# Performance work log

Hardware: AMD Instinct MI355X
Metric: run time of the kernel (lower is better)

Reference implementation:

```python
import jax, jax.numpy as jnp
import numpy as np
import math

FACTOR = 5  # Informer 'factor' hyperparameter


def setup_inputs() -> dict:
    key = jax.random.key(0)
    B, L, H, D = 2, 2048, 16, 128
    k1, k2, k3, k4 = jax.random.split(key, 4)
    queries = jax.random.normal(k1, (B, L, H, D), jnp.float32)
    keys = jax.random.normal(k2, (B, L, H, D), jnp.float32)
    values = jax.random.normal(k3, (B, L, H, D), jnp.float32)
    sample_k = max(1, min(FACTOR * math.ceil(math.log(L)), L))  # u in the paper
    index_sample = jax.random.randint(k4, (L, sample_k), 0, L, dtype=jnp.int32)
    return {"queries": queries, "keys": keys, "values": values,
            "index_sample": index_sample}


def reference(queries, keys, values, index_sample):
    # queries/keys/values: [B, L, H, D] -> [B, H, L, D]
    Q = jnp.swapaxes(queries, 1, 2)
    K = jnp.swapaxes(keys, 1, 2)
    V = jnp.swapaxes(values, 1, 2)
    B, H, L_Q, D = Q.shape
    L_K = K.shape[2]
    # U_part = factor*ceil(ln L_K), clipped to L_K then to L_Q (n_top in _prob_QK)
    n_top = max(1, min(FACTOR * math.ceil(math.log(L_K)), L_K, L_Q))

    # --- _prob_QK: sampled scores ---
    # K_sample: [B, H, L_Q, sample_k, D] (same materialization as torch K_expand gather)
    K_sample = K[:, :, index_sample, :]
    Q_K_sample = jnp.einsum('bhqd,bhqsd->bhqs', Q, K_sample)
    # sparsity measure M: max - mean(over full L_K, per original torch code)
    M = Q_K_sample.max(axis=-1) - Q_K_sample.sum(axis=-1) / L_K  # [B,H,L_Q]
    _, M_top = jax.lax.top_k(M, n_top)  # [B,H,n_top]

    # gather top queries and compute their full attention rows
    Q_reduce = jnp.take_along_axis(Q, M_top[..., None], axis=2)  # [B,H,u,D]
    scores = jnp.einsum('bhud,bhkd->bhuk', Q_reduce, K)  # [B,H,u,L_K]
    scale = 1.0 / math.sqrt(D)
    scores = scores * scale

    # --- initial context (mask_flag=False): mean of V over keys ---
    context = jnp.broadcast_to(V.mean(axis=2, keepdims=True), (B, H, L_Q, D))

    # --- update context at top-query positions ---
    attn = jax.nn.softmax(scores, axis=-1)
    upd = jnp.einsum('bhuk,bhkd->bhud', attn, V)  # [B,H,u,D]
    bi = jnp.arange(B)[:, None, None]
    hi = jnp.arange(H)[None, :, None]
    context = context.at[bi, hi, M_top].set(upd)

    return jnp.swapaxes(context, 1, 2)  # [B, L_Q, H, D]
```

## Files before the change

kernel.cpp:

```cpp
#include <hip/hip_runtime.h>
#include <math.h>

#define B_    2
#define L_    2048
#define H_    16
#define D_    128
#define S_    40
#define NTOP_ 40
#define NCH_  8
#define CHK_  256
#define VCH_  32

#define SCALE_ 0.08838834764831843f

#define NVP_BLKS   1024
#define NSAMP_BLKS 16384

__global__ __launch_bounds__(256) void k1_sample_vpart(const float* __restrict__ Q,
                                                       const float* __restrict__ K,
                                                       const float* __restrict__ V,
                                                       const int* __restrict__ idx,
                                                       float* __restrict__ M,
                                                       float* __restrict__ vpart,
                                                       int* __restrict__ cnt) {
    const int bid = blockIdx.x;
    const int t   = threadIdx.x;

    if (bid < NVP_BLKS) {
        __shared__ float red[256];
        if (bid == 0 && t < 32) cnt[t] = 0;
        const int vbid = bid;
        const int bh  = vbid >> 5;
        const int lc  = vbid & (VCH_ - 1);
        const int h   = bh & (H_ - 1);
        const int b   = bh >> 4;
        const int d   = t & (D_ - 1);
        const int sub = t >> 7;
        float acc = 0.0f;
        const int l0 = lc * (L_ / VCH_);
        for (int l = l0 + sub; l < l0 + L_ / VCH_; l += 2)
            acc += V[((size_t)(b * L_ + l) * H_ + h) * D_ + d];
        red[t] = acc;
        __syncthreads();
        if (t < D_) vpart[(size_t)vbid * D_ + t] = red[t] + red[t + 128];
        return;
    }

    const int sb   = bid - NVP_BLKS;
    const int xcd  = sb & 7;
    const int li   = sb >> 3;
    const int bh   = (xcd << 2) + (li >> 9);
    const int rb   = li & 511;
    const int wave = t >> 6;
    const int lane = t & 63;
    const int q    = rb * 4 + wave;
    const int h    = bh & (H_ - 1);
    const int b    = bh >> 4;
    const int g    = lane >> 3;
    const int sub  = lane & 7;

    const float4* Q4 = (const float4*)Q;
    const float4* K4 = (const float4*)K;
    const size_t rowQ = ((size_t)(b * L_ + q) * H_ + h) * 32;
    const size_t kbase = ((size_t)b * L_ * H_ + h) * 32 + sub;
    const int* ip = idx + q * S_;

    int kidx[5];
    #pragma unroll
    for (int s = 0; s < 5; ++s) kidx[s] = ip[s * 8 + g];

    const float4 qv0 = Q4[rowQ + 0  + sub];
    const float4 qv1 = Q4[rowQ + 8  + sub];
    const float4 qv2 = Q4[rowQ + 16 + sub];
    const float4 qv3 = Q4[rowQ + 24 + sub];

    float4 kv[5][4];
    #pragma unroll
    for (int s = 0; s < 5; ++s) {
        const float4* kb = K4 + kbase + (size_t)kidx[s] * (H_ * 32);
        kv[s][0] = kb[0];
        kv[s][1] = kb[8];
        kv[s][2] = kb[16];
        kv[s][3] = kb[24];
    }
    __builtin_amdgcn_sched_barrier(0);

    float smax = -INFINITY, ssum = 0.0f;
    #pragma unroll
    for (int s = 0; s < 5; ++s) {
        float p = qv0.x * kv[s][0].x + qv0.y * kv[s][0].y + qv0.z * kv[s][0].z + qv0.w * kv[s][0].w
                + qv1.x * kv[s][1].x + qv1.y * kv[s][1].y + qv1.z * kv[s][1].z + qv1.w * kv[s][1].w
                + qv2.x * kv[s][2].x + qv2.y * kv[s][2].y + qv2.z * kv[s][2].z + qv2.w * kv[s][2].w
                + qv3.x * kv[s][3].x + qv3.y * kv[s][3].y + qv3.z * kv[s][3].z + qv3.w * kv[s][3].w;
        p += __shfl_xor(p, 1);
        p += __shfl_xor(p, 2);
        p += __shfl_xor(p, 4);
        smax = fmaxf(smax, p);
        ssum += p;
    }
    #pragma unroll
    for (int o = 8; o < 64; o <<= 1) {
        smax = fmaxf(smax, __shfl_xor(smax, o));
        ssum += __shfl_xor(ssum, o);
    }
    if (lane == 0) M[(size_t)bh * L_ + q] = smax - ssum * (1.0f / L_);
}

__global__ __launch_bounds__(256) void k2_rank_fill(const float* __restrict__ M,
                                                    const float* __restrict__ vpart,
                                                    int* __restrict__ cnt,
                                                    int* __restrict__ topk,
                                                    float* __restrict__ out) {
    __shared__ unsigned int ue[L_];
    __shared__ int hist[256], sscan[256];
    __shared__ int eqlist[256];
    __shared__ int sh_chosen, sh_need, sh_eqcnt;
    __shared__ float mlf[256];
    const int bid = blockIdx.x;
    const int t   = threadIdx.x;

    if (bid < 32) {
        const int bh = bid;
        const float* Mrow = M + (size_t)bh * L_;
        for (int i = t; i < L_; i += 256) {
            const unsigned int ub = __float_as_uint(Mrow[i]);
            ue[i] = (ub & 0x80000000u) ? ~ub : (ub | 0x80000000u);
        }
        if (t == 0) sh_eqcnt = 0;
        __syncthreads();

        unsigned int prefix = 0;
        int need = NTOP_;
        for (int l = 3; l >= 0; --l) {
            hist[t] = 0;
            __syncthreads();
            for (int i = t; i < L_; i += 256) {
                const unsigned int u = ue[i];
                const bool match = (l == 3) || ((u >> (8 * (l + 1))) == prefix);
                if (match) atomicAdd(&hist[(u >> (8 * l)) & 255], 1);
            }
            __syncthreads();
            sscan[t] = hist[t];
            __syncthreads();
            for (int off = 1; off < 256; off <<= 1) {
                const int v = (t + off < 256) ? sscan[t + off] : 0;
                __syncthreads();
                sscan[t] += v;
                __syncthreads();
            }
            const int above = sscan[t] - hist[t];
            if (above < need && need <= above + hist[t]) {
                sh_chosen = t;
                sh_need = need - above;
            }
            __syncthreads();
            prefix = (prefix << 8) | (unsigned int)sh_chosen;
            need = sh_need;
            __syncthreads();
        }
        const unsigned int T40 = prefix;
        const int rem = need;

        for (int i = t; i < L_; i += 256) {
            const unsigned int u = ue[i];
            if (u > T40) {
                const int pos = atomicAdd(&cnt[bh], 1);
                topk[bh * NTOP_ + pos] = i;
            } else if (u == T40) {
                const int p = atomicAdd(&sh_eqcnt, 1);
                if (p < 256) eqlist[p] = i;
            }
        }
        __syncthreads();
        const int n = min(sh_eqcnt, 256);
        for (int i = t; i < n; i += 256) {
            const int mye = eqlist[i];
            int rk = 0;
            for (int j = 0; j < n; ++j) rk += (eqlist[j] < mye);
            if (rk < rem) {
                const int pos = atomicAdd(&cnt[bh], 1);
                topk[bh * NTOP_ + pos] = mye;
            }
        }
    } else {
        const int fb = bid - 32;
        const int bh = fb >> 6;
        const int sl = fb & 63;
        const int h  = bh & (H_ - 1);
        const int b  = bh >> 4;
        const int d    = t & (D_ - 1);
        const int half = t >> 7;
        float s = 0.0f;
        #pragma unroll
        for (int c = half * 16; c < half * 16 + 16; ++c)
            s += vpart[(size_t)(bh * VCH_ + c) * D_ + d];
        mlf[t] = s;
        __syncthreads();
        if (t < D_) mlf[t] = (mlf[t] + mlf[t + 128]) * (1.0f / L_);
        __syncthreads();
        const float4 vm4 = *(const float4*)&mlf[(t & 31) * 4];
        float4* out4 = (float4*)out;
        const int q0 = sl * 32;
        #pragma unroll
        for (int k = 0; k < 4; ++k) {
            const int j = k * 256 + t;
            const int r = j >> 5;
            out4[((size_t)(b * L_ + q0 + r) * H_ + h) * 32 + (t & 31)] = vm4;
        }
    }
}

__global__ __launch_bounds__(256) void k_scorepv(const float* __restrict__ Q,
                                                 const float* __restrict__ K,
                                                 const float* __restrict__ V,
                                                 const int* __restrict__ topk,
                                                 float* __restrict__ pmax,
                                                 float* __restrict__ psum,
                                                 float* __restrict__ pout) {
    __shared__ float Qs[20 * D_];
    __shared__ float S[20 * 260];
    __shared__ float Ks[64 * 132];
    __shared__ float mrow[20];
    __shared__ int   tq[20];
    const int bid = blockIdx.x;
    const int xcd = bid & 7;
    const int loc = bid >> 3;
    const int bh  = (xcd << 2) + (loc >> 4);
    const int sub16 = loc & 15;
    const int kc  = sub16 >> 1;
    const int uh  = sub16 & 1;
    const int h   = bh & (H_ - 1);
    const int b   = bh >> 4;
    const int t   = threadIdx.x;

    if (t < 20) tq[t] = topk[bh * NTOP_ + uh * 20 + t];
    __syncthreads();

    {
        const float4* Q4 = (const float4*)Q;
        float4* Qs4 = (float4*)Qs;
        #pragma unroll
        for (int it = 0; it < 3; ++it) {
            const int i = it * 256 + t;
            if (i < 640) {
                const int u = i >> 5, dc = i & 31;
                Qs4[i] = Q4[((size_t)(b * L_ + tq[u]) * H_ + h) * 32 + dc];
            }
        }
    }
    __syncthreads();

    {
        const float4* K4 = (const float4*)K;
        const float4* Qs4 = (const float4*)Qs;
        float4* Ks4 = (float4*)Ks;
        const int r = t & 63, uq = t >> 6;
        for (int pass = 0; pass < 4; ++pass) {
            #pragma unroll
            for (int j = 0; j < 8; ++j) {
                const int gidx = j * 256 + t;
                const int row = gidx >> 5, c = gidx & 31;
                Ks4[row * 33 + c] =
                    K4[((size_t)(b * L_ + kc * CHK_ + pass * 64 + row) * H_ + h) * 32 + c];
            }
            __syncthreads();
            float acc[5] = {0.f, 0.f, 0.f, 0.f, 0.f};
            for (int dc = 0; dc < 32; ++dc) {
                const float4 kv = Ks4[r * 33 + dc];
                #pragma unroll
                for (int u5 = 0; u5 < 5; ++u5) {
                    const float4 qv = Qs4[(uq * 5 + u5) * 32 + dc];
                    acc[u5] += qv.x * kv.x + qv.y * kv.y + qv.z * kv.z + qv.w * kv.w;
                }
            }
            #pragma unroll
            for (int u5 = 0; u5 < 5; ++u5)
                S[(uq * 5 + u5) * 260 + pass * 64 + r] = acc[u5] * SCALE_;
            __syncthreads();
        }
    }

    {
        const int w = t >> 6, lane = t & 63;
        #pragma unroll
        for (int uu = 0; uu < 5; ++uu) {
            const int u = w * 5 + uu;
            const float* Sr = S + u * 260;
            float v = fmaxf(fmaxf(Sr[lane], Sr[lane + 64]),
                            fmaxf(Sr[lane + 128], Sr[lane + 192]));
            #pragma unroll
            for (int o = 1; o < 64; o <<= 1) v = fmaxf(v, __shfl_xor(v, o, 64));
            if (lane == 0) mrow[u] = v;
        }
    }
    __syncthreads();

    #pragma unroll
    for (int u = 0; u < 20; ++u) S[u * 260 + t] = __expf(S[u * 260 + t] - mrow[u]);
    __syncthreads();

    {
        const int w = t >> 6, lane = t & 63;
        #pragma unroll
        for (int uu = 0; uu < 5; ++uu) {
            const int u = w * 5 + uu;
            const float* Sr = S + u * 260;
            float v = Sr[lane] + Sr[lane + 64] + Sr[lane + 128] + Sr[lane + 192];
            #pragma unroll
            for (int o = 1; o < 64; o <<= 1) v += __shfl_xor(v, o, 64);
            if (lane == 0) {
                psum[(bh * NCH_ + kc) * NTOP_ + uh * 20 + u] = v;
                pmax[(bh * NCH_ + kc) * NTOP_ + uh * 20 + u] = mrow[u];
            }
        }
    }

    {
        const int d  = t & (D_ - 1);
        const int g  = t >> 7;
        const int u0 = g * 10;
        float acc2[10];
        #pragma unroll
        for (int u = 0; u < 10; ++u) acc2[u] = 0.0f;
        const float* Vb = V + ((size_t)(b * L_ + kc * CHK_) * H_ + h) * D_ + d;
        for (int kq = 0; kq < CHK_ / 4; ++kq) {
            const float v0 = Vb[(size_t)(kq * 4 + 0) * (H_ * D_)];
            const float v1 = Vb[(size_t)(kq * 4 + 1) * (H_ * D_)];
            const float v2 = Vb[(size_t)(kq * 4 + 2) * (H_ * D_)];
            const float v3 = Vb[(size_t)(kq * 4 + 3) * (H_ * D_)];
            #pragma unroll
            for (int u = 0; u < 10; ++u) {
                const float4 p = *(const float4*)&S[(u0 + u) * 260 + kq * 4];
                acc2[u] += p.x * v0 + p.y * v1 + p.z * v2 + p.w * v3;
            }
        }
        float* pb = pout + (((size_t)(bh * NCH_ + kc)) * NTOP_ + uh * 20 + u0) * D_ + d;
        #pragma unroll
        for (int u = 0; u < 10; ++u) pb[(size_t)u * D_] = acc2[u];
    }
}

__global__ __launch_bounds__(128) void k_comb(const float* __restrict__ pmax,
                                              const float* __restrict__ psum,
                                              const float* __restrict__ pout,
                                              const int* __restrict__ topk,
                                              float* __restrict__ out) {
    const int bid = blockIdx.x;
    const int bh  = bid / NTOP_;
    const int u   = bid - bh * NTOP_;
    const int h   = bh & (H_ - 1);
    const int b   = bh >> 4;
    const int t   = threadIdx.x;

    float pm[NCH_];
    float M = -INFINITY;
    #pragma unroll
    for (int c = 0; c < NCH_; ++c) {
        pm[c] = pmax[(bh * NCH_ + c) * NTOP_ + u];
        M = fmaxf(M, pm[c]);
    }
    float ssum = 0.0f, o = 0.0f;
    #pragma unroll
    for (int c = 0; c < NCH_; ++c) {
        const float w = __expf(pm[c] - M);
        ssum += psum[(bh * NCH_ + c) * NTOP_ + u] * w;
        o += pout[((size_t)(bh * NCH_ + c) * NTOP_ + u) * D_ + t] * w;
    }
    const int qi = topk[bh * NTOP_ + u];
    out[((size_t)(b * L_ + qi) * H_ + h) * D_ + t] = o / ssum;
}

extern "C" void kernel_launch(void* const* d_in, const int* in_sizes, int n_in,
                              void* d_out, int out_size, void* d_ws, size_t ws_size,
                              hipStream_t stream) {
    const float* Q  = (const float*)d_in[0];
    const float* K  = (const float*)d_in[1];
    const float* V  = (const float*)d_in[2];
    const int* idx  = (const int*)d_in[3];
    float* out      = (float*)d_out;

    char* ws = (char*)d_ws;
    size_t off = 0;
    float* Mws   = (float*)(ws + off); off += (size_t)65536 * 4;
    float* vpart = (float*)(ws + off); off += (size_t)1024 * 128 * 4;
    int*   cnt   = (int*)(ws + off);   off += 32 * 4;
    int*   topk  = (int*)(ws + off);   off += 1280 * 4;
    float* pmax  = (float*)(ws + off); off += (size_t)256 * 40 * 4;
    float* psum  = (float*)(ws + off); off += (size_t)256 * 40 * 4;
    float* pout  = (float*)(ws + off); off += (size_t)256 * 40 * 128 * 4;

    hipLaunchKernelGGL(k1_sample_vpart, dim3(NVP_BLKS + NSAMP_BLKS), dim3(256), 0, stream,
                       Q, K, V, idx, Mws, vpart, cnt);
    hipLaunchKernelGGL(k2_rank_fill,    dim3(32 + 2048), dim3(256), 0, stream,
                       Mws, vpart, cnt, topk, out);
    hipLaunchKernelGGL(k_scorepv,       dim3(512),  dim3(256), 0, stream,
                       Q, K, V, topk, pmax, psum, pout);
    hipLaunchKernelGGL(k_comb,          dim3(1280), dim3(128), 0, stream,
                       pmax, psum, pout, topk, out);
}
```

Before: 135.8 us.

## Score sampled keys in bf16, then refine top-k candidates with exact fp32

```diff
diff --git a/kernel.cpp b/kernel.cpp
--- a/kernel.cpp
+++ b/kernel.cpp
@@ -10,81 +10,157 @@
 #define NCH_  8
 #define CHK_  256
 #define VCH_  32
+#define CAND_ 512
 
 #define SCALE_ 0.08838834764831843f
 
-#define NVP_BLKS   1024
-#define NSAMP_BLKS 16384
-
-__global__ __launch_bounds__(256) void k1_sample_vpart(const float* __restrict__ Q,
-                                                       const float* __restrict__ K,
-                                                       const float* __restrict__ V,
-                                                       const int* __restrict__ idx,
-                                                       float* __restrict__ M,
-                                                       float* __restrict__ vpart,
-                                                       int* __restrict__ cnt) {
-    const int bid = blockIdx.x;
+__device__ __forceinline__ unsigned int encf(float f) {
+    unsigned int u = __float_as_uint(f);
+    return (u & 0x80000000u) ? ~u : (u | 0x80000000u);
+}
+__device__ __forceinline__ float decf(unsigned int e) {
+    unsigned int u = (e & 0x80000000u) ? (e ^ 0x80000000u) : ~e;
+    return __uint_as_float(u);
+}
+__device__ __forceinline__ unsigned int bfpack(float a, float b) {
+    unsigned int ua = __float_as_uint(a); ua = (ua + 0x7fffu + ((ua >> 16) & 1u)) >> 16;
+    unsigned int ub = __float_as_uint(b); ub = (ub + 0x7fffu + ((ub >> 16) & 1u)) >> 16;
+    return ua | (ub << 16);
+}
+__device__ __forceinline__ float lo16(unsigned int u) { return __uint_as_float(u << 16); }
+__device__ __forceinline__ float hi16(unsigned int u) { return __uint_as_float(u & 0xffff0000u); }
+
+__global__ __launch_bounds__(256) void kpack(const float* __restrict__ K,
+                                             unsigned int* __restrict__ Kbf) {
+    const int bid = blockIdx.x, t = threadIdx.x;
+    const int bh = bid >> 3, kc = bid & 7;
+    const int h = bh & 15, b = bh >> 4;
+    const float4* K4 = (const float4*)K;
+    uint2* out2 = (uint2*)Kbf;
+    for (int j = 0; j < 32; ++j) {
+        const int g = j * 256 + t;
+        const int row = g >> 5, c = g & 31;
+        const float4 v = K4[((size_t)(b * L_ + kc * 256 + row) * H_ + h) * 32 + c];
+        out2[(size_t)(bh * L_ + kc * 256 + row) * 32 + c] =
+            make_uint2(bfpack(v.x, v.y), bfpack(v.z, v.w));
+    }
+}
+
+__global__ __launch_bounds__(256) void k0_vpart(const float* __restrict__ V,
+                                                float* __restrict__ vpart) {
+    __shared__ float red[256];
+    const int vbid = blockIdx.x;
+    const int bh  = vbid >> 5;
+    const int lc  = vbid & (VCH_ - 1);
+    const int h   = bh & 15, b = bh >> 4;
     const int t   = threadIdx.x;
-
-    if (bid < NVP_BLKS) {
-        __shared__ float red[256];
-        if (bid == 0 && t < 32) cnt[t] = 0;
-        const int vbid = bid;
-        const int bh  = vbid >> 5;
-        const int lc  = vbid & (VCH_ - 1);
-        const int h   = bh & (H_ - 1);
-        const int b   = bh >> 4;
-        const int d   = t & (D_ - 1);
-        const int sub = t >> 7;
-        float acc = 0.0f;
-        const int l0 = lc * (L_ / VCH_);
-        for (int l = l0 + sub; l < l0 + L_ / VCH_; l += 2)
-            acc += V[((size_t)(b * L_ + l) * H_ + h) * D_ + d];
-        red[t] = acc;
-        __syncthreads();
-        if (t < D_) vpart[(size_t)vbid * D_ + t] = red[t] + red[t + 128];
-        return;
-    }
-
-    const int sb   = bid - NVP_BLKS;
+    const int d   = t & (D_ - 1);
+    const int sub = t >> 7;
+    float acc = 0.0f;
+    const int l0 = lc * (L_ / VCH_);
+    for (int l = l0 + sub; l < l0 + L_ / VCH_; l += 2)
+        acc += V[((size_t)(b * L_ + l) * H_ + h) * D_ + d];
+    red[t] = acc;
+    __syncthreads();
+    if (t < D_) vpart[(size_t)vbid * D_ + t] = red[t] + red[t + 128];
+}
+
+__global__ __launch_bounds__(256) void k1_sample_bf16(const float* __restrict__ Q,
+                                                      const uint4* __restrict__ KB,
+                                                      const int* __restrict__ idx,
+                                                      float* __restrict__ M) {
+    const int sb   = blockIdx.x;
     const int xcd  = sb & 7;
     const int li   = sb >> 3;
     const int bh   = (xcd << 2) + (li >> 9);
     const int rb   = li & 511;
-    const int wave = t >> 6;
-    const int lane = t & 63;
+    const int wave = threadIdx.x >> 6, lane = threadIdx.x & 63;
     const int q    = rb * 4 + wave;
-    const int h    = bh & (H_ - 1);
-    const int b    = bh >> 4;
-    const int g    = lane >> 3;
-    const int sub  = lane & 7;
+    const int h    = bh & 15, b = bh >> 4;
+    const int g    = lane >> 3, sub = lane & 7;
+
+    const float4* Q4 = (const float4*)Q;
+    const size_t rowQ = ((size_t)(b * L_ + q) * H_ + h) * 32;
+    const int* ip = idx + q * S_;
+    int kidx[5];
+    #pragma unroll
+    for (int s = 0; s < 5; ++s) kidx[s] = ip[s * 8 + g];
+
+    const float4 qa0 = Q4[rowQ + 2 * sub];
+    const float4 qa1 = Q4[rowQ + 2 * sub + 1];
+    const float4 qb0 = Q4[rowQ + 16 + 2 * sub];
+    const float4 qb1 = Q4[rowQ + 16 + 2 * sub + 1];
+
+    uint4 kv[5][2];
+    #pragma unroll
+    for (int s = 0; s < 5; ++s) {
+        const uint4* kr = KB + ((size_t)bh * L_ + kidx[s]) * 16;
+        kv[s][0] = kr[sub];
+        kv[s][1] = kr[8 + sub];
+    }
+    __builtin_amdgcn_sched_barrier(0);
+
+    float smax = -INFINITY, ssum = 0.0f;
+    #pragma unroll
+    for (int s = 0; s < 5; ++s) {
+        float p = 0.f;
+        {
+            const uint4 u = kv[s][0];
+            p += qa0.x * lo16(u.x) + qa0.y * hi16(u.x) + qa0.z * lo16(u.y) + qa0.w * hi16(u.y);
+            p += qa1.x * lo16(u.z) + qa1.y * hi16(u.z) + qa1.z * lo16(u.w) + qa1.w * hi16(u.w);
+        }
+        {
+            const uint4 u = kv[s][1];
+            p += qb0.x * lo16(u.x) + qb0.y * hi16(u.x) + qb0.z * lo16(u.y) + qb0.w * hi16(u.y);
+            p += qb1.x * lo16(u.z) + qb1.y * hi16(u.z) + qb1.z * lo16(u.w) + qb1.w * hi16(u.w);
+        }
+        p += __shfl_xor(p, 1);
+        p += __shfl_xor(p, 2);
+        p += __shfl_xor(p, 4);
+        smax = fmaxf(smax, p);
+        ssum += p;
+    }
+    #pragma unroll
+    for (int o = 8; o < 64; o <<= 1) {
+        smax = fmaxf(smax, __shfl_xor(smax, o));
+        ssum += __shfl_xor(ssum, o);
+    }
+    if (lane == 0) M[(size_t)bh * L_ + q] = smax - ssum * (1.0f / L_);
+}
+
+__global__ __launch_bounds__(256) void k1_sample_f32(const float* __restrict__ Q,
+                                                     const float* __restrict__ K,
+                                                     const int* __restrict__ idx,
+                                                     float* __restrict__ M) {
+    const int sb   = blockIdx.x;
+    const int xcd  = sb & 7;
+    const int li   = sb >> 3;
+    const int bh   = (xcd << 2) + (li >> 9);
+    const int rb   = li & 511;
+    const int wave = threadIdx.x >> 6, lane = threadIdx.x & 63;
+    const int q    = rb * 4 + wave;
+    const int h    = bh & 15, b = bh >> 4;
+    const int g    = lane >> 3, sub = lane & 7;
 
     const float4* Q4 = (const float4*)Q;
     const float4* K4 = (const float4*)K;
     const size_t rowQ = ((size_t)(b * L_ + q) * H_ + h) * 32;
     const size_t kbase = ((size_t)b * L_ * H_ + h) * 32 + sub;
     const int* ip = idx + q * S_;
-
     int kidx[5];
     #pragma unroll
     for (int s = 0; s < 5; ++s) kidx[s] = ip[s * 8 + g];
-
-    const float4 qv0 = Q4[rowQ + 0  + sub];
-    const float4 qv1 = Q4[rowQ + 8  + sub];
+    const float4 qv0 = Q4[rowQ + 0 + sub];
+    const float4 qv1 = Q4[rowQ + 8 + sub];
     const float4 qv2 = Q4[rowQ + 16 + sub];
     const float4 qv3 = Q4[rowQ + 24 + sub];
-
     float4 kv[5][4];
     #pragma unroll
     for (int s = 0; s < 5; ++s) {
         const float4* kb = K4 + kbase + (size_t)kidx[s] * (H_ * 32);
-        kv[s][0] = kb[0];
-        kv[s][1] = kb[8];
-        kv[s][2] = kb[16];
-        kv[s][3] = kb[24];
+        kv[s][0] = kb[0]; kv[s][1] = kb[8]; kv[s][2] = kb[16]; kv[s][3] = kb[24];
     }
     __builtin_amdgcn_sched_barrier(0);
-
     float smax = -INFINITY, ssum = 0.0f;
     #pragma unroll
     for (int s = 0; s < 5; ++s) {
@@ -106,106 +182,133 @@
     if (lane == 0) M[(size_t)bh * L_ + q] = smax - ssum * (1.0f / L_);
 }
 
-__global__ __launch_bounds__(256) void k2_rank_fill(const float* __restrict__ M,
-                                                    const float* __restrict__ vpart,
-                                                    int* __restrict__ cnt,
-                                                    int* __restrict__ topk,
-                                                    float* __restrict__ out) {
-    __shared__ unsigned int ue[L_];
-    __shared__ int hist[256], sscan[256];
-    __shared__ int eqlist[256];
-    __shared__ int sh_chosen, sh_need, sh_eqcnt;
-    __shared__ float mlf[256];
-    const int bid = blockIdx.x;
-    const int t   = threadIdx.x;
-
+__global__ __launch_bounds__(1024) void k2_rank_refine_fill(const float* __restrict__ Mws,
+                                                            const float* __restrict__ Q,
+                                                            const float* __restrict__ K,
+                                                            const int* __restrict__ idx,
+                                                            const float* __restrict__ vpart,
+                                                            int* __restrict__ topk,
+                                                            float* __restrict__ out,
+                                                            float delta) {
+    const int bid = blockIdx.x, t = threadIdx.x;
     if (bid < 32) {
-        const int bh = bid;
-        const float* Mrow = M + (size_t)bh * L_;
-        for (int i = t; i < L_; i += 256) {
-            const unsigned int ub = __float_as_uint(Mrow[i]);
-            ue[i] = (ub & 0x80000000u) ? ~ub : (ub | 0x80000000u);
-        }
-        if (t == 0) sh_eqcnt = 0;
-        __syncthreads();
-
-        unsigned int prefix = 0;
-        int need = NTOP_;
+        __shared__ unsigned int ue[L_];
+        __shared__ int hist[256], sscan[256];
+        __shared__ int sh_chosen, sh_need, sh_nc;
+        __shared__ int clist[CAND_];
+        __shared__ float cMx[CAND_];
+        __shared__ unsigned int cmaxe[CAND_];
+        __shared__ float csum[CAND_];
+        const int bh = bid, h = bh & 15, b = bh >> 4;
+        const float* Mrow = Mws + (size_t)bh * L_;
+        for (int i = t; i < L_; i += 1024) ue[i] = encf(Mrow[i]);
+        if (t == 0) sh_nc = 0;
+        __syncthreads();
+
+        unsigned int prefix = 0; int need = NTOP_;
         for (int l = 3; l >= 0; --l) {
-            hist[t] = 0;
-            __syncthreads();
-            for (int i = t; i < L_; i += 256) {
+            if (t < 256) hist[t] = 0;
+            __syncthreads();
+            for (int i = t; i < L_; i += 1024) {
                 const unsigned int u = ue[i];
                 const bool match = (l == 3) || ((u >> (8 * (l + 1))) == prefix);
                 if (match) atomicAdd(&hist[(u >> (8 * l)) & 255], 1);
             }
             __syncthreads();
-            sscan[t] = hist[t];
+            if (t < 256) sscan[t] = hist[t];
             __syncthreads();
             for (int off = 1; off < 256; off <<= 1) {
-                const int v = (t + off < 256) ? sscan[t + off] : 0;
+                int v = 0;
+                if (t < 256 && t + off < 256) v = sscan[t + off];
                 __syncthreads();
-                sscan[t] += v;
+                if (t < 256) sscan[t] += v;
                 __syncthreads();
             }
-            const int above = sscan[t] - hist[t];
-            if (above < need && need <= above + hist[t]) {
-                sh_chosen = t;
-                sh_need = need - above;
+            if (t < 256) {
+                const int above = sscan[t] - hist[t];
+                if (above < need && need <= above + hist[t]) { sh_chosen = t; sh_need = need - above; }
             }
             __syncthreads();
             prefix = (prefix << 8) | (unsigned int)sh_chosen;
             need = sh_need;
             __syncthreads();
         }
-        const unsigned int T40 = prefix;
-        const int rem = need;
-
-        for (int i = t; i < L_; i += 256) {
-            const unsigned int u = ue[i];
-            if (u > T40) {
-                const int pos = atomicAdd(&cnt[bh], 1);
-                topk[bh * NTOP_ + pos] = i;
-            } else if (u == T40) {
-                const int p = atomicAdd(&sh_eqcnt, 1);
-                if (p < 256) eqlist[p] = i;
-            }
-        }
-        __syncthreads();
-        const int n = min(sh_eqcnt, 256);
-        for (int i = t; i < n; i += 256) {
-            const int mye = eqlist[i];
+        const unsigned int ethr = encf(decf(prefix) - delta);
+        for (int i = t; i < L_; i += 1024) {
+            if (ue[i] >= ethr) {
+                const int p = atomicAdd(&sh_nc, 1);
+                if (p < CAND_) clist[p] = i;
+            }
+        }
+        __syncthreads();
+        const int nc = min(sh_nc, CAND_);
+        for (int i = t; i < CAND_; i += 1024) { cmaxe[i] = 0x007FFFFFu; csum[i] = 0.f; }
+        __syncthreads();
+
+        const float4* Q4 = (const float4*)Q;
+        const float4* K4 = (const float4*)K;
+        const int grp = t >> 3, sub = t & 7;
+        for (int task = grp; task < nc * S_; task += 128) {
+            const int ci = task / S_;
+            const int s  = task - ci * S_;
+            const int qq = clist[ci];
+            const int ki = idx[qq * S_ + s];
+            const float4* Kr = K4 + ((size_t)(b * L_ + ki) * H_ + h) * 32;
+            const float4* Qr = Q4 + ((size_t)(b * L_ + qq) * H_ + h) * 32;
+            float p = 0.f;
+            #pragma unroll
+            for (int qt2 = 0; qt2 < 4; ++qt2) {
+                const float4 kv = Kr[qt2 * 8 + sub];
+                const float4 qv = Qr[qt2 * 8 + sub];
+                p += qv.x * kv.x + qv.y * kv.y + qv.z * kv.z + qv.w * kv.w;
+            }
+            p += __shfl_xor(p, 1);
+            p += __shfl_xor(p, 2);
+            p += __shfl_xor(p, 4);
+            if (sub == 0) {
+                atomicMax(&cmaxe[ci], encf(p));
+                atomicAdd(&csum[ci], p);
+            }
+        }
+        __syncthreads();
+        if (t < nc) cMx[t] = decf(cmaxe[t]) - csum[t] * (1.0f / L_);
+        __syncthreads();
+        if (t < nc) {
+            const float mi = cMx[t]; const int qi = clist[t];
             int rk = 0;
-            for (int j = 0; j < n; ++j) rk += (eqlist[j] < mye);
-            if (rk < rem) {
-                const int pos = atomicAdd(&cnt[bh], 1);
-                topk[bh * NTOP_ + pos] = mye;
-            }
+            for (int j = 0; j < nc; ++j) {
+                const float mj = cMx[j];
+                rk += (mj > mi) || (mj == mi && clist[j] < qi);
+            }
+            if (rk < NTOP_) topk[bh * NTOP_ + rk] = qi;
         }
     } else {
+        __shared__ float red[1024];
+        __shared__ float vmf[128];
         const int fb = bid - 32;
-        const int bh = fb >> 6;
-        const int sl = fb & 63;
-        const int h  = bh & (H_ - 1);
-        const int b  = bh >> 4;
-        const int d    = t & (D_ - 1);
-        const int half = t >> 7;
-        float s = 0.0f;
-        #pragma unroll
-        for (int c = half * 16; c < half * 16 + 16; ++c)
+        const int bh = fb >> 4, sl = fb & 15;
+        const int h = bh & 15, b = bh >> 4;
+        const int d = t & 127, grp = t >> 7;
+        float s = 0.f;
+        #pragma unroll
+        for (int c = grp * 4; c < grp * 4 + 4; ++c)
             s += vpart[(size_t)(bh * VCH_ + c) * D_ + d];
-        mlf[t] = s;
-        __syncthreads();
-        if (t < D_) mlf[t] = (mlf[t] + mlf[t + 128]) * (1.0f / L_);
-        __syncthreads();
-        const float4 vm4 = *(const float4*)&mlf[(t & 31) * 4];
+        red[t] = s;
+        __syncthreads();
+        if (t < 512) red[t] += red[t + 512];
+        __syncthreads();
+        if (t < 256) red[t] += red[t + 256];
+        __syncthreads();
+        if (t < 128) vmf[t] = (red[t] + red[t + 128]) * (1.0f / L_);
+        __syncthreads();
+        const float4 vm4 = *(const float4*)&vmf[(t & 31) * 4];
         float4* out4 = (float4*)out;
-        const int q0 = sl * 32;
+        const int q0 = sl * 128;
         #pragma unroll
         for (int k = 0; k < 4; ++k) {
-            const int j = k * 256 + t;
-            const int r = j >> 5;
-            out4[((size_t)(b * L_ + q0 + r) * H_ + h) * 32 + (t & 31)] = vm4;
+            const int j = k * 1024 + t;
+            const int r = j >> 5, c = j & 31;
+            out4[((size_t)(b * L_ + q0 + r) * H_ + h) * 32 + c] = vm4;
         }
     }
 }
@@ -229,8 +332,7 @@
     const int sub16 = loc & 15;
     const int kc  = sub16 >> 1;
     const int uh  = sub16 & 1;
-    const int h   = bh & (H_ - 1);
-    const int b   = bh >> 4;
+    const int h   = bh & 15, b = bh >> 4;
     const int t   = threadIdx.x;
 
     if (t < 20) tq[t] = topk[bh * NTOP_ + uh * 20 + t];
@@ -348,8 +450,7 @@
     const int bid = blockIdx.x;
     const int bh  = bid / NTOP_;
     const int u   = bid - bh * NTOP_;
-    const int h   = bh & (H_ - 1);
-    const int b   = bh >> 4;
+    const int h   = bh & 15, b = bh >> 4;
     const int t   = threadIdx.x;
 
     float pm[NCH_];
@@ -383,18 +484,27 @@
     size_t off = 0;
     float* Mws   = (float*)(ws + off); off += (size_t)65536 * 4;
     float* vpart = (float*)(ws + off); off += (size_t)1024 * 128 * 4;
-    int*   cnt   = (int*)(ws + off);   off += 32 * 4;
     int*   topk  = (int*)(ws + off);   off += 1280 * 4;
     float* pmax  = (float*)(ws + off); off += (size_t)256 * 40 * 4;
     float* psum  = (float*)(ws + off); off += (size_t)256 * 40 * 4;
     float* pout  = (float*)(ws + off); off += (size_t)256 * 40 * 128 * 4;
-
-    hipLaunchKernelGGL(k1_sample_vpart, dim3(NVP_BLKS + NSAMP_BLKS), dim3(256), 0, stream,
-                       Q, K, V, idx, Mws, vpart, cnt);
-    hipLaunchKernelGGL(k2_rank_fill,    dim3(32 + 2048), dim3(256), 0, stream,
-                       Mws, vpart, cnt, topk, out);
-    hipLaunchKernelGGL(k_scorepv,       dim3(512),  dim3(256), 0, stream,
+    unsigned int* Kbf = (unsigned int*)(ws + off);
+    const size_t kbf_bytes = (size_t)32 * L_ * D_ * 2;
+    const bool use_bf16 = (ws_size >= off + kbf_bytes);
+
+    if (use_bf16)
+        hipLaunchKernelGGL(kpack, dim3(256), dim3(256), 0, stream, K, Kbf);
+    hipLaunchKernelGGL(k0_vpart, dim3(1024), dim3(256), 0, stream, V, vpart);
+    if (use_bf16)
+        hipLaunchKernelGGL(k1_sample_bf16, dim3(16384), dim3(256), 0, stream,
+                           Q, (const uint4*)Kbf, idx, Mws);
+    else
+        hipLaunchKernelGGL(k1_sample_f32, dim3(16384), dim3(256), 0, stream,
+                           Q, K, idx, Mws);
+    hipLaunchKernelGGL(k2_rank_refine_fill, dim3(32 + 512), dim3(1024), 0, stream,
+                       Mws, Q, K, idx, vpart, topk, out, use_bf16 ? 2.0f : 0.01f);
+    hipLaunchKernelGGL(k_scorepv, dim3(512), dim3(256), 0, stream,
                        Q, K, V, topk, pmax, psum, pout);
-    hipLaunchKernelGGL(k_comb,          dim3(1280), dim3(128), 0, stream,
+    hipLaunchKernelGGL(k_comb, dim3(1280), dim3(128), 0, stream,
                        pmax, psum, pout, topk, out);
 }
```

Result: slower. 153.6 us (+13.1%).
